# Kernel tuning notes

Measured on AMD Instinct MI355X. Metric: run time of the kernel, lower is better.

The kernel has to match this reference:

```python
import jax, jax.numpy as jnp
import numpy as np

BS, J, N, C, C_OUT = 4, 4, 2000, 32, 32
BN_EPS = 1e-5

def setup_inputs() -> dict:
    key = jax.random.key(0)
    k1, k2, k3 = jax.random.split(key, 3)
    W = jax.random.normal(k1, (BS, J, N, N), dtype=jnp.float32)
    x = jax.random.normal(k2, (BS, C, N, 1), dtype=jnp.float32)
    gamma = jnp.ones((J * C,), dtype=jnp.float32)
    beta = jnp.zeros((J * C,), dtype=jnp.float32)
    # 1x1 Conv2d(J*C -> C_OUT): kernel reduces to a [C_OUT, J*C] matrix
    fan_in = J * C
    bound = 1.0 / np.sqrt(fan_in)
    conv_w = jax.random.uniform(k3, (C_OUT, J * C), dtype=jnp.float32, minval=-bound, maxval=bound)
    conv_b = jnp.zeros((C_OUT,), dtype=jnp.float32)
    return {"W": W, "x": x, "gamma": gamma, "beta": beta, "conv_w": conv_w, "conv_b": conv_b}

def reference(W, x, gamma, beta, conv_w, conv_b):
    bs, j, n, _ = W.shape
    c = x.shape[1]
    # gmul: apply each of the J operators to x, concat on channel dim
    # y[b, j*c + ci, m, w] = sum_n W[b,j,m,n] * x[b,ci,n,w]
    y = jnp.einsum('bjmn,bcnw->bjcmw', W, x).reshape(bs, j * c, n, -1)
    # BatchNorm2d (training-mode batch statistics) over (batch, H, W) per channel
    mean = jnp.mean(y, axis=(0, 2, 3), keepdims=True)
    var = jnp.var(y, axis=(0, 2, 3), keepdims=True)
    yn = (y - mean) * jax.lax.rsqrt(var + BN_EPS)
    yn = yn * gamma[None, :, None, None] + beta[None, :, None, None]
    # activation then 1x1 conv (a GEMM over channels)
    ya = jax.nn.relu(yn)
    out = jnp.einsum('oc,bcnw->bonw', conv_w, ya) + conv_b[None, :, None, None]
    return out
```

## Files before the change

kernel.cpp:

```cpp
#include <hip/hip_runtime.h>

typedef short bf16x8 __attribute__((ext_vector_type(8)));
typedef float f32x4 __attribute__((ext_vector_type(4)));

#define NBJ 16
#define NMT 125
#define NKT 63
#define NCH 128
#define NM  2000
#define NB  4
#define NJ  4
#define NC  32
#define BN_EPS 1e-5f

__device__ inline void bf16_split(float v, short& hi, short& lo) {
    unsigned u = __float_as_uint(v);
    unsigned rn = (u + 0x7fffu + ((u >> 16) & 1u)) & 0xffff0000u;
    hi = (short)(rn >> 16);
    float d = v - __uint_as_float(rn);
    unsigned ud = __float_as_uint(d);
    lo = (short)((ud + 0x7fffu + ((ud >> 16) & 1u)) >> 16);
}

__global__ __launch_bounds__(256) void prep_kernel(
        const float* __restrict__ x, short* __restrict__ xfrag,
        float* __restrict__ csum ) {
    int gid = blockIdx.x * 256 + threadIdx.x;
    if (gid < 256) csum[gid] = 0.f;
    int lane = gid & 63;
    int t = gid >> 6;
    int ct = t & 1; t >>= 1;
    int kt = t % NKT;
    int b  = t / NKT;
    int c  = ct * 16 + (lane & 15);
    int k0 = kt * 32 + (lane >> 4) * 8;
    const float* xp = x + ((size_t)b * NC + c) * NM;
    bf16x8 hi, lo;
#pragma unroll
    for (int j = 0; j < 8; ++j) {
        int k = k0 + j;
        float v = (k < NM) ? xp[k] : 0.f;
        short h, l;
        bf16_split(v, h, l);
        hi[j] = h; lo[j] = l;
    }
    size_t base = ((((size_t)b * NKT + kt) * 2 + ct) * 2) * 512 + (size_t)lane * 8;
    *(bf16x8*)(xfrag + base)       = hi;
    *(bf16x8*)(xfrag + base + 512) = lo;
}

__global__ __launch_bounds__(256) void gemm_kernel(
        const float* __restrict__ W, const short* __restrict__ xfrag,
        float* __restrict__ y, float* __restrict__ csum, float* __restrict__ csumsq) {
    const int lane = threadIdx.x & 63;
    const int wid  = (blockIdx.x << 2) + (threadIdx.x >> 6);
    const int bj = wid / NMT;
    const int mt = wid - bj * NMT;
    const int b  = bj >> 2;
    const int quad = lane >> 4;
    const int r = lane & 15;

    const float* wp = W + ((size_t)bj * NM + mt * 16 + r) * NM + quad * 8;
    const short* xb = xfrag + (size_t)b * NKT * 2048;
    const int loff = lane * 8;

    f32x4 acc0 = {0.f, 0.f, 0.f, 0.f};
    f32x4 acc1 = {0.f, 0.f, 0.f, 0.f};

#define BFRAG(kt, ct, hl) (*(const bf16x8*)(xb + (size_t)(kt) * 2048 + (ct) * 1024 + (hl) * 512 + loff))

    float4 a0c, a1c;
    bf16x8 bh0c, bl0c, bh1c, bl1c;
    a0c = *(const float4*)(wp);
    a1c = *(const float4*)(wp + 4);
    bh0c = BFRAG(0, 0, 0); bl0c = BFRAG(0, 0, 1);
    bh1c = BFRAG(0, 1, 0); bl1c = BFRAG(0, 1, 1);

    for (int kt = 0; kt < NKT; ++kt) {
        float4 a0n, a1n;
        bf16x8 bh0n, bl0n, bh1n, bl1n;
        const int ktn = kt + 1;
        if (ktn < NKT) {
            const float4 z4 = make_float4(0.f, 0.f, 0.f, 0.f);
            a0n = z4; a1n = z4;
            if ((ktn < NKT - 1) | (quad < 2)) {
                const float* wpn = wp + ktn * 32;
                a0n = *(const float4*)(wpn);
                a1n = *(const float4*)(wpn + 4);
            }
            bh0n = BFRAG(ktn, 0, 0); bl0n = BFRAG(ktn, 0, 1);
            bh1n = BFRAG(ktn, 1, 0); bl1n = BFRAG(ktn, 1, 1);
        }
        bf16x8 ah, al;
        float v[8] = {a0c.x, a0c.y, a0c.z, a0c.w, a1c.x, a1c.y, a1c.z, a1c.w};
#pragma unroll
        for (int j = 0; j < 8; ++j) {
            short h, l;
            bf16_split(v[j], h, l);
            ah[j] = h; al[j] = l;
        }
        acc0 = __builtin_amdgcn_mfma_f32_16x16x32_bf16(ah, bh0c, acc0, 0, 0, 0);
        acc1 = __builtin_amdgcn_mfma_f32_16x16x32_bf16(ah, bh1c, acc1, 0, 0, 0);
        acc0 = __builtin_amdgcn_mfma_f32_16x16x32_bf16(al, bh0c, acc0, 0, 0, 0);
        acc1 = __builtin_amdgcn_mfma_f32_16x16x32_bf16(al, bh1c, acc1, 0, 0, 0);
        acc0 = __builtin_amdgcn_mfma_f32_16x16x32_bf16(ah, bl0c, acc0, 0, 0, 0);
        acc1 = __builtin_amdgcn_mfma_f32_16x16x32_bf16(ah, bl1c, acc1, 0, 0, 0);
        if (ktn < NKT) {
            a0c = a0n; a1c = a1n;
            bh0c = bh0n; bl0c = bl0n; bh1c = bh1n; bl1c = bl1n;
        }
    }

    float s0 = acc0[0] + acc0[1] + acc0[2] + acc0[3];
    float q0 = acc0[0]*acc0[0] + acc0[1]*acc0[1] + acc0[2]*acc0[2] + acc0[3]*acc0[3];
    float s1 = acc1[0] + acc1[1] + acc1[2] + acc1[3];
    float q1 = acc1[0]*acc1[0] + acc1[1]*acc1[1] + acc1[2]*acc1[2] + acc1[3]*acc1[3];
    s0 += __shfl_xor(s0, 16); s0 += __shfl_xor(s0, 32);
    q0 += __shfl_xor(q0, 16); q0 += __shfl_xor(q0, 32);
    s1 += __shfl_xor(s1, 16); s1 += __shfl_xor(s1, 32);
    q1 += __shfl_xor(q1, 16); q1 += __shfl_xor(q1, 32);
    const int j = bj & 3;
    if (quad == 0) {
        atomicAdd(&csum[j * NC + r], s0);
        atomicAdd(&csumsq[j * NC + r], q0);
        atomicAdd(&csum[j * NC + 16 + r], s1);
        atomicAdd(&csumsq[j * NC + 16 + r], q1);
    }

    float* yp = y + ((size_t)bj * NM + mt * 16 + quad * 4) * NC + r;
#pragma unroll
    for (int i = 0; i < 4; ++i) {
        yp[i * NC]      = acc0[i];
        yp[i * NC + 16] = acc1[i];
    }
}

__global__ __launch_bounds__(256) void conv_kernel(
        const float* __restrict__ y, const float* __restrict__ csum,
        const float* __restrict__ csumsq, const float* __restrict__ gamma,
        const float* __restrict__ beta, const float* __restrict__ conv_w,
        const float* __restrict__ conv_b, float* __restrict__ out) {
    __shared__ float wt[NCH * 32];
    __shared__ float sscale[NCH], sshift[NCH], scb[32];
    const int t = threadIdx.x;
    if (t < NCH) {
        const float inv = 1.f / (NB * NM);
        float mean = csum[t] * inv;
        float var = csumsq[t] * inv - mean * mean;
        var = fmaxf(var, 0.f);
        float rs = rsqrtf(var + BN_EPS);
        float sc = gamma[t] * rs;
        sscale[t] = sc;
        sshift[t] = beta[t] - mean * sc;
    }
    if (t < 32) scb[t] = conv_b[t];
#pragma unroll
    for (int i = t; i < NCH * 32; i += 256)
        wt[i] = conv_w[(i & 31) * NCH + (i >> 5)];
    __syncthreads();

    int g = blockIdx.x * 256 + t;
    int oq = g & 3;
    int bm = g >> 2;
    int m = bm % NM;
    int b = bm / NM;

    float acc[8];
#pragma unroll
    for (int u = 0; u < 8; ++u) acc[u] = scb[oq * 8 + u];

#pragma unroll
    for (int jj = 0; jj < NJ; ++jj) {
        const float4* y4 = (const float4*)(y + (((size_t)b * NJ + jj) * NM + m) * NC);
#pragma unroll
        for (int q = 0; q < 8; ++q) {
            float4 v = y4[q];
            int jc = jj * NC + q * 4;
            float ya0 = fmaxf(fmaf(v.x, sscale[jc],     sshift[jc]),     0.f);
            float ya1 = fmaxf(fmaf(v.y, sscale[jc + 1], sshift[jc + 1]), 0.f);
            float ya2 = fmaxf(fmaf(v.z, sscale[jc + 2], sshift[jc + 2]), 0.f);
            float ya3 = fmaxf(fmaf(v.w, sscale[jc + 3], sshift[jc + 3]), 0.f);
#pragma unroll
            for (int u = 0; u < 8; ++u) {
                int o = oq * 8 + u;
                acc[u] = fmaf(ya0, wt[(jc)     * 32 + o], acc[u]);
                acc[u] = fmaf(ya1, wt[(jc + 1) * 32 + o], acc[u]);
                acc[u] = fmaf(ya2, wt[(jc + 2) * 32 + o], acc[u]);
                acc[u] = fmaf(ya3, wt[(jc + 3) * 32 + o], acc[u]);
            }
        }
    }
#pragma unroll
    for (int u = 0; u < 8; ++u)
        out[((size_t)b * 32 + oq * 8 + u) * NM + m] = acc[u];
}

extern "C" void kernel_launch(void* const* d_in, const int* in_sizes, int n_in,
                              void* d_out, int out_size, void* d_ws, size_t ws_size,
                              hipStream_t stream) {
    const float* W      = (const float*)d_in[0];
    const float* x      = (const float*)d_in[1];
    const float* gamma  = (const float*)d_in[2];
    const float* beta   = (const float*)d_in[3];
    const float* conv_w = (const float*)d_in[4];
    const float* conv_b = (const float*)d_in[5];
    float* out = (float*)d_out;

    char* ws = (char*)d_ws;
    float* y      = (float*)ws;
    float* csum   = (float*)(ws + 4096000);
    float* csumsq = (float*)(ws + 4096512);
    short* xfrag  = (short*)(ws + 4097024);

    prep_kernel<<<126, 256, 0, stream>>>(x, xfrag, csum);
    gemm_kernel<<<500, 256, 0, stream>>>(W, xfrag, y, csum, csumsq);
    conv_kernel<<<125, 256, 0, stream>>>(y, csum, csumsq, gamma, beta, conv_w, conv_b, out);
}
```

Measured before the change: 376.0 us.

## Deepen W prefetch to two tiles and restage conv kernel through shared memory

The GEMM loop now prefetches W fragments two K-tiles ahead instead of one, so more global loads are in flight to hide latency on the W stream, which dominates memory traffic. The conv kernel is restructured so each block stages a 32-row tile of normalized, ReLU'd activations in padded shared memory. Threads then compute 4 outputs each with coalesced output stores, and the grid roughly doubles. This costs extra registers in the GEMM and extra shared memory and a barrier in the conv kernel.

```diff
diff --git a/kernel.cpp b/kernel.cpp
--- a/kernel.cpp
+++ b/kernel.cpp
@@ -49,6 +49,17 @@
     *(bf16x8*)(xfrag + base + 512) = lo;
 }
 
+__device__ inline void loadA(const float* __restrict__ wp, int t, int quad,
+                             float4& a0, float4& a1) {
+    float4 z = make_float4(0.f, 0.f, 0.f, 0.f);
+    a0 = z; a1 = z;
+    if ((t < NKT - 1) | (quad < 2)) {
+        const float* p = wp + (size_t)t * 32;
+        a0 = *(const float4*)p;
+        a1 = *(const float4*)(p + 4);
+    }
+}
+
 __global__ __launch_bounds__(256) void gemm_kernel(
         const float* __restrict__ W, const short* __restrict__ xfrag,
         float* __restrict__ y, float* __restrict__ csum, float* __restrict__ csumsq) {
@@ -69,45 +80,41 @@
 
 #define BFRAG(kt, ct, hl) (*(const bf16x8*)(xb + (size_t)(kt) * 2048 + (ct) * 1024 + (hl) * 512 + loff))
 
-    float4 a0c, a1c;
-    bf16x8 bh0c, bl0c, bh1c, bl1c;
-    a0c = *(const float4*)(wp);
-    a1c = *(const float4*)(wp + 4);
-    bh0c = BFRAG(0, 0, 0); bl0c = BFRAG(0, 0, 1);
-    bh1c = BFRAG(0, 1, 0); bl1c = BFRAG(0, 1, 1);
+    float4 c00, c01, c10, c11;
+    loadA(wp, 0, quad, c00, c01);
+    loadA(wp, 1, quad, c10, c11);
+    bf16x8 bh0 = BFRAG(0, 0, 0), bl0 = BFRAG(0, 0, 1);
+    bf16x8 bh1 = BFRAG(0, 1, 0), bl1 = BFRAG(0, 1, 1);
 
     for (int kt = 0; kt < NKT; ++kt) {
-        float4 a0n, a1n;
-        bf16x8 bh0n, bl0n, bh1n, bl1n;
-        const int ktn = kt + 1;
-        if (ktn < NKT) {
-            const float4 z4 = make_float4(0.f, 0.f, 0.f, 0.f);
-            a0n = z4; a1n = z4;
-            if ((ktn < NKT - 1) | (quad < 2)) {
-                const float* wpn = wp + ktn * 32;
-                a0n = *(const float4*)(wpn);
-                a1n = *(const float4*)(wpn + 4);
-            }
-            bh0n = BFRAG(ktn, 0, 0); bl0n = BFRAG(ktn, 0, 1);
-            bh1n = BFRAG(ktn, 1, 0); bl1n = BFRAG(ktn, 1, 1);
+        float4 c20, c21;
+        if (kt + 2 < NKT) {
+            loadA(wp, kt + 2, quad, c20, c21);
+        } else {
+            c20 = make_float4(0.f, 0.f, 0.f, 0.f); c21 = c20;
+        }
+        bf16x8 nh0, nl0, nh1, nl1;
+        if (kt + 1 < NKT) {
+            nh0 = BFRAG(kt + 1, 0, 0); nl0 = BFRAG(kt + 1, 0, 1);
+            nh1 = BFRAG(kt + 1, 1, 0); nl1 = BFRAG(kt + 1, 1, 1);
         }
         bf16x8 ah, al;
-        float v[8] = {a0c.x, a0c.y, a0c.z, a0c.w, a1c.x, a1c.y, a1c.z, a1c.w};
+        float v[8] = {c00.x, c00.y, c00.z, c00.w, c01.x, c01.y, c01.z, c01.w};
 #pragma unroll
         for (int j = 0; j < 8; ++j) {
             short h, l;
             bf16_split(v[j], h, l);
             ah[j] = h; al[j] = l;
         }
-        acc0 = __builtin_amdgcn_mfma_f32_16x16x32_bf16(ah, bh0c, acc0, 0, 0, 0);
-        acc1 = __builtin_amdgcn_mfma_f32_16x16x32_bf16(ah, bh1c, acc1, 0, 0, 0);
-        acc0 = __builtin_amdgcn_mfma_f32_16x16x32_bf16(al, bh0c, acc0, 0, 0, 0);
-        acc1 = __builtin_amdgcn_mfma_f32_16x16x32_bf16(al, bh1c, acc1, 0, 0, 0);
-        acc0 = __builtin_amdgcn_mfma_f32_16x16x32_bf16(ah, bl0c, acc0, 0, 0, 0);
-        acc1 = __builtin_amdgcn_mfma_f32_16x16x32_bf16(ah, bl1c, acc1, 0, 0, 0);
-        if (ktn < NKT) {
-            a0c = a0n; a1c = a1n;
-            bh0c = bh0n; bl0c = bl0n; bh1c = bh1n; bl1c = bl1n;
+        acc0 = __builtin_amdgcn_mfma_f32_16x16x32_bf16(ah, bh0, acc0, 0, 0, 0);
+        acc1 = __builtin_amdgcn_mfma_f32_16x16x32_bf16(ah, bh1, acc1, 0, 0, 0);
+        acc0 = __builtin_amdgcn_mfma_f32_16x16x32_bf16(al, bh0, acc0, 0, 0, 0);
+        acc1 = __builtin_amdgcn_mfma_f32_16x16x32_bf16(al, bh1, acc1, 0, 0, 0);
+        acc0 = __builtin_amdgcn_mfma_f32_16x16x32_bf16(ah, bl0, acc0, 0, 0, 0);
+        acc1 = __builtin_amdgcn_mfma_f32_16x16x32_bf16(ah, bl1, acc1, 0, 0, 0);
+        c00 = c10; c01 = c11; c10 = c20; c11 = c21;
+        if (kt + 1 < NKT) {
+            bh0 = nh0; bl0 = nl0; bh1 = nh1; bl1 = nl1;
         }
     }
 
@@ -135,14 +142,19 @@
     }
 }
 
+#define MT 32
 __global__ __launch_bounds__(256) void conv_kernel(
         const float* __restrict__ y, const float* __restrict__ csum,
         const float* __restrict__ csumsq, const float* __restrict__ gamma,
         const float* __restrict__ beta, const float* __restrict__ conv_w,
         const float* __restrict__ conv_b, float* __restrict__ out) {
+    __shared__ float ya[MT][NCH + 1];
     __shared__ float wt[NCH * 32];
     __shared__ float sscale[NCH], sshift[NCH], scb[32];
     const int t = threadIdx.x;
+    const int b  = blockIdx.x & 3;
+    const int m0 = (blockIdx.x >> 2) * MT;
+
     if (t < NCH) {
         const float inv = 1.f / (NB * NM);
         float mean = csum[t] * inv;
@@ -159,40 +171,44 @@
         wt[i] = conv_w[(i & 31) * NCH + (i >> 5)];
     __syncthreads();
 
-    int g = blockIdx.x * 256 + t;
-    int oq = g & 3;
-    int bm = g >> 2;
-    int m = bm % NM;
-    int b = bm / NM;
-
-    float acc[8];
-#pragma unroll
-    for (int u = 0; u < 8; ++u) acc[u] = scb[oq * 8 + u];
-
-#pragma unroll
-    for (int jj = 0; jj < NJ; ++jj) {
-        const float4* y4 = (const float4*)(y + (((size_t)b * NJ + jj) * NM + m) * NC);
-#pragma unroll
-        for (int q = 0; q < 8; ++q) {
-            float4 v = y4[q];
-            int jc = jj * NC + q * 4;
-            float ya0 = fmaxf(fmaf(v.x, sscale[jc],     sshift[jc]),     0.f);
-            float ya1 = fmaxf(fmaf(v.y, sscale[jc + 1], sshift[jc + 1]), 0.f);
-            float ya2 = fmaxf(fmaf(v.z, sscale[jc + 2], sshift[jc + 2]), 0.f);
-            float ya3 = fmaxf(fmaf(v.w, sscale[jc + 3], sshift[jc + 3]), 0.f);
-#pragma unroll
-            for (int u = 0; u < 8; ++u) {
-                int o = oq * 8 + u;
-                acc[u] = fmaf(ya0, wt[(jc)     * 32 + o], acc[u]);
-                acc[u] = fmaf(ya1, wt[(jc + 1) * 32 + o], acc[u]);
-                acc[u] = fmaf(ya2, wt[(jc + 2) * 32 + o], acc[u]);
-                acc[u] = fmaf(ya3, wt[(jc + 3) * 32 + o], acc[u]);
-            }
-        }
-    }
-#pragma unroll
-    for (int u = 0; u < 8; ++u)
-        out[((size_t)b * 32 + oq * 8 + u) * NM + m] = acc[u];
+#pragma unroll
+    for (int i = t; i < 1024; i += 256) {
+        int jj = i >> 8;
+        int e  = (i & 255) * 4;
+        int ml = e >> 5, c = e & 31;
+        int m  = m0 + ml;
+        float4 v = make_float4(0.f, 0.f, 0.f, 0.f);
+        if (m < NM)
+            v = *(const float4*)(y + (((size_t)b * NJ + jj) * NM + m) * NC + c);
+        int jc = jj * 32 + c;
+        ya[ml][jc    ] = fmaxf(fmaf(v.x, sscale[jc    ], sshift[jc    ]), 0.f);
+        ya[ml][jc + 1] = fmaxf(fmaf(v.y, sscale[jc + 1], sshift[jc + 1]), 0.f);
+        ya[ml][jc + 2] = fmaxf(fmaf(v.z, sscale[jc + 2], sshift[jc + 2]), 0.f);
+        ya[ml][jc + 3] = fmaxf(fmaf(v.w, sscale[jc + 3], sshift[jc + 3]), 0.f);
+    }
+    __syncthreads();
+
+    const int o_hi = t >> 5;
+    const int ml   = t & 31;
+    float acc[4];
+#pragma unroll
+    for (int u = 0; u < 4; ++u) acc[u] = scb[o_hi * 4 + u];
+
+#pragma unroll 4
+    for (int jc = 0; jc < NCH; ++jc) {
+        float v = ya[ml][jc];
+        float4 w4 = *(const float4*)&wt[jc * 32 + o_hi * 4];
+        acc[0] = fmaf(v, w4.x, acc[0]);
+        acc[1] = fmaf(v, w4.y, acc[1]);
+        acc[2] = fmaf(v, w4.z, acc[2]);
+        acc[3] = fmaf(v, w4.w, acc[3]);
+    }
+    int m = m0 + ml;
+    if (m < NM) {
+#pragma unroll
+        for (int u = 0; u < 4; ++u)
+            out[((size_t)b * 32 + o_hi * 4 + u) * NM + m] = acc[u];
+    }
 }
 
 extern "C" void kernel_launch(void* const* d_in, const int* in_sizes, int n_in,
@@ -214,5 +230,5 @@
 
     prep_kernel<<<126, 256, 0, stream>>>(x, xfrag, csum);
     gemm_kernel<<<500, 256, 0, stream>>>(W, xfrag, y, csum, csumsq);
-    conv_kernel<<<125, 256, 0, stream>>>(y, csum, csumsq, gamma, beta, conv_w, conv_b, out);
-}
+    conv_kernel<<<252, 256, 0, stream>>>(y, csum, csumsq, gamma, beta, conv_w, conv_b, out);
+}
```

Result: slower. 386.5 us (+2.8%).
